# Kernel tuning notes

Measured on AMD Instinct MI355X. Metric: run time of the kernel, lower is better.

## Reference

```python
import jax, jax.numpy as jnp
import numpy as np

N = 8192
D = 256  # hidden_size = in_features = out_features
NEG_SLOPE = 0.01  # nn.LeakyReLU() default
MASK_VAL = -1e12


def setup_inputs() -> dict:
    key = jax.random.key(0)
    k1, k2, k3, k4 = jax.random.split(key, 4)
    x = jax.random.normal(k1, (N, D), dtype=jnp.float32)
    adj = jax.random.randint(k2, (N, N), 0, 2, dtype=jnp.int32)
    # kaiming_uniform_ style params (scaled random uniform)
    W = jax.random.normal(k3, (D, D), dtype=jnp.float32) * (1.0 / np.sqrt(D))
    a = jax.random.normal(k4, (2 * D, 1), dtype=jnp.float32) * (1.0 / np.sqrt(2 * D))
    return {"x": x, "adj": adj, "W": W, "a": a}


def reference(x, adj, W, a):
    # GraphAttentionLayer.forward (eval mode: dropout is identity)
    h = x @ W  # [N, D]
    # a_input[i,j] = concat(h_i, h_j); a_input @ a decomposes as:
    #   e[i,j] = h_i . a[:D] + h_j . a[D:]
    # identical math without materializing the [N, N, 2D] tensor.
    e_src = h @ a[:D, 0]  # [N]
    e_dst = h @ a[D:, 0]  # [N]
    e = e_src[:, None] + e_dst[None, :]  # [N, N]
    e = jnp.where(e > 0, e, NEG_SLOPE * e)  # LeakyReLU
    att_logits = jnp.where(adj > 0, e, MASK_VAL)
    attention = jax.nn.softmax(att_logits, axis=1)
    h_prime = attention @ h  # [N, D]
    return jax.nn.elu(h_prime)  # concat=True branch
```

## Files before the change

### kernel.cpp

```cpp
#include <hip/hip_runtime.h>

#define NN 8192
#define DD 256
#define JSPLIT 2
#define JCH (NN / JSPLIT)
#define NSTEP (JCH / 32)

typedef __attribute__((ext_vector_type(8))) short short8;
typedef __attribute__((ext_vector_type(4))) float f32x4;

__device__ __forceinline__ short f2bf(float x) {
    union { float f; unsigned u; } v; v.f = x;
    unsigned r = (v.u + 0x7FFFu + ((v.u >> 16) & 1u)) >> 16;
    return (short)r;
}
__device__ __forceinline__ float bf2f(short b) {
    union { float f; unsigned u; } v; v.u = ((unsigned)(unsigned short)b) << 16;
    return v.f;
}

__device__ __forceinline__ void barrier_keep_vmem() {
    asm volatile("s_waitcnt lgkmcnt(0)" ::: "memory");
    __builtin_amdgcn_s_barrier();
    asm volatile("" ::: "memory");
}

__global__ __launch_bounds__(256) void gat_prep(
    const float* __restrict__ x, const float* __restrict__ W,
    const float* __restrict__ a,
    short* __restrict__ hT, float* __restrict__ e_src, float* __restrict__ e_dst)
{
    __shared__ float x_s[32][260];
    __shared__ float W_s[2][16][256];
    const int t  = threadIdx.x;
    const int ib = blockIdx.x * 32;

    #pragma unroll
    for (int rep = 0; rep < 8; ++rep) {
        int fi = rep * 256 + t;
        int r  = fi >> 6;
        int c4 = (fi & 63) * 4;
        float4 v = *(const float4*)(x + (size_t)(ib + r) * DD + c4);
        *(float4*)&x_s[r][c4] = v;
    }
    float4 wp[4];
    #pragma unroll
    for (int q = 0; q < 4; ++q) {
        int fi = q * 256 + t;
        wp[q] = *(const float4*)(W + (size_t)(fi >> 6) * DD + (fi & 63) * 4);
    }
    barrier_keep_vmem();

    const int il = t >> 3;
    const int dg = (t & 7) * 4;
    f32x4 acc[8];
    #pragma unroll
    for (int m = 0; m < 8; ++m) acc[m] = (f32x4){0.f, 0.f, 0.f, 0.f};

    for (int kc = 0; kc < 16; ++kc) {
        const int b = kc & 1;
        #pragma unroll
        for (int q = 0; q < 4; ++q) {
            int fi = q * 256 + t;
            *(float4*)&W_s[b][fi >> 6][(fi & 63) * 4] = wp[q];
        }
        if (kc < 15) {
            #pragma unroll
            for (int q = 0; q < 4; ++q) {
                int fi = q * 256 + t;
                wp[q] = *(const float4*)(W + (size_t)((kc + 1) * 16 + (fi >> 6)) * DD + (fi & 63) * 4);
            }
        }
        barrier_keep_vmem();
        #pragma unroll
        for (int kl = 0; kl < 16; ++kl) {
            float xv = x_s[il][kc * 16 + kl];
            #pragma unroll
            for (int m = 0; m < 8; ++m) {
                float4 wv = *(const float4*)&W_s[b][kl][m * 32 + dg];
                acc[m].x += xv * wv.x; acc[m].y += xv * wv.y;
                acc[m].z += xv * wv.z; acc[m].w += xv * wv.w;
            }
        }
    }

    const int ig = ib + il;
    float p1 = 0.f, p2 = 0.f;
    #pragma unroll
    for (int m = 0; m < 8; ++m) {
        #pragma unroll
        for (int j = 0; j < 4; ++j) {
            int col = m * 32 + dg + j;
            float hv = acc[m][j];
            p1 += hv * a[col];
            p2 += hv * a[DD + col];
            hT[(size_t)col * NN + ig] = f2bf(hv);
        }
    }
    p1 += __shfl_xor(p1, 1); p1 += __shfl_xor(p1, 2); p1 += __shfl_xor(p1, 4);
    p2 += __shfl_xor(p2, 1); p2 += __shfl_xor(p2, 2); p2 += __shfl_xor(p2, 4);
    if ((t & 7) == 0) { e_src[ig] = p1; e_dst[ig] = p2; }
}

__global__ __launch_bounds__(512, 4) void gat_main(
    const int* __restrict__ adj, const short* __restrict__ hT,
    const float* __restrict__ e_src, const float* __restrict__ e_dst,
    float* __restrict__ num0, float* __restrict__ num1,
    float* __restrict__ den_part)
{
    __shared__ __align__(16) short w_s[2][32][40];

    const int t    = threadIdx.x;
    const int lane = t & 63;
    const int wid  = t >> 6;
    const int ibl  = (blockIdx.x >> 1) * 32;
    const int half = blockIdx.x & 1;
    const int jb   = half * JCH;

    const int irow = t >> 4;
    const int jc2  = (t & 15) * 2;
    const float es = e_src[ibl + irow];
    const int* adj_row = adj + (size_t)(ibl + irow) * NN + jb;
    const float* edp = e_dst + jb;

    const int cb   = wid * 32;
    const int arow = lane & 15;
    const int kg8  = (lane >> 4) * 8;
    const short* hB = hT + (size_t)(cb + arow) * NN + jb + kg8;

    float dsum = 0.f;
    f32x4 acc00 = {0.f,0.f,0.f,0.f}, acc01 = acc00, acc10 = acc00, acc11 = acc00;

    int2   adA = *(const int2*)(adj_row + jc2);
    float2 edA = *(const float2*)(edp + jc2);
    int4   b0A = *(const int4*)(hB);
    int4   b1A = *(const int4*)(hB + 16 * NN);
    int2   adB = *(const int2*)(adj_row + 32 + jc2);
    float2 edB = *(const float2*)(edp + 32 + jc2);
    int4   b0B = *(const int4*)(hB + 32);
    int4   b1B = *(const int4*)(hB + 16 * NN + 32);

#define MAIN_STEP(AD, ED, B0, B1, n)                                           \
    {                                                                          \
        const int c = (n) & 1;                                                 \
        int4 g0 = B0, g1 = B1;                       \
        float s0 = es + ED.x, s1 = es + ED.y;                                  \
        float l0 = s0 > 0.f ? s0 : 0.01f * s0;                                 \
        float l1 = s1 > 0.f ? s1 : 0.01f * s1;                                 \
        float w0 = AD.x > 0 ? __expf(l0) : 0.f;                                \
        float w1 = AD.y > 0 ? __expf(l1) : 0.f;                                \
        short b0 = f2bf(w0), b1 = f2bf(w1);                                    \
        dsum += bf2f(b0) + bf2f(b1);    \
        *(unsigned*)&w_s[c][irow][jc2] =                                       \
            (unsigned)(unsigned short)b0 | ((unsigned)(unsigned short)b1 << 16);\
        int jn = (((n) + 2) & (NSTEP - 1)) * 32;         \
        AD = *(const int2*)(adj_row + jn + jc2);                               \
        ED = *(const float2*)(edp + jn + jc2);                                 \
        B0 = *(const int4*)(hB + jn);                                          \
        B1 = *(const int4*)(hB + 16 * NN + jn);                                \
        barrier_keep_vmem();          \
        short8 a0 = *(const short8*)&w_s[c][arow][kg8];                        \
        short8 a1 = *(const short8*)&w_s[c][16 + arow][kg8];                   \
        acc00 = __builtin_amdgcn_mfma_f32_16x16x32_bf16(a0, *(short8*)&g0, acc00, 0, 0, 0);\
        acc01 = __builtin_amdgcn_mfma_f32_16x16x32_bf16(a0, *(short8*)&g1, acc01, 0, 0, 0);\
        acc10 = __builtin_amdgcn_mfma_f32_16x16x32_bf16(a1, *(short8*)&g0, acc10, 0, 0, 0);\
        acc11 = __builtin_amdgcn_mfma_f32_16x16x32_bf16(a1, *(short8*)&g1, acc11, 0, 0, 0);\
    }

    for (int n = 0; n < NSTEP; n += 2) {
        MAIN_STEP(adA, edA, b0A, b1A, n)
        MAIN_STEP(adB, edB, b0B, b1B, n + 1)
    }
#undef MAIN_STEP

    dsum += __shfl_xor(dsum, 1);
    dsum += __shfl_xor(dsum, 2);
    dsum += __shfl_xor(dsum, 4);
    dsum += __shfl_xor(dsum, 8);
    if ((t & 15) == 0) den_part[half * NN + ibl + irow] = dsum;

    float* num = half ? num1 : num0;
    const int r4 = (lane >> 4) * 4;
    #pragma unroll
    for (int r = 0; r < 4; ++r) {
        size_t o0 = (size_t)(ibl + r4 + r) * DD + cb + arow;
        size_t o1 = (size_t)(ibl + 16 + r4 + r) * DD + cb + arow;
        num[o0]      = acc00[r];
        num[o0 + 16] = acc01[r];
        num[o1]      = acc10[r];
        num[o1 + 16] = acc11[r];
    }
}

__global__ __launch_bounds__(256) void gat_epi(
    float* __restrict__ out, const float* __restrict__ num1,
    const float* __restrict__ den_part)
{
    int idx = blockIdx.x * 256 + threadIdx.x;
    int row = idx >> 6;
    float inv = 1.f / (den_part[row] + den_part[NN + row]);
    float4 p0 = ((const float4*)out)[idx];
    float4 p1 = ((const float4*)num1)[idx];
    float4 v;
    v.x = (p0.x + p1.x) * inv; v.x = v.x > 0.f ? v.x : expm1f(v.x);
    v.y = (p0.y + p1.y) * inv; v.y = v.y > 0.f ? v.y : expm1f(v.y);
    v.z = (p0.z + p1.z) * inv; v.z = v.z > 0.f ? v.z : expm1f(v.z);
    v.w = (p0.w + p1.w) * inv; v.w = v.w > 0.f ? v.w : expm1f(v.w);
    ((float4*)out)[idx] = v;
}

extern "C" void kernel_launch(void* const* d_in, const int* in_sizes, int n_in,
                              void* d_out, int out_size, void* d_ws, size_t ws_size,
                              hipStream_t stream) {
    const float* x   = (const float*)d_in[0];
    const int*   adj = (const int*)d_in[1];
    const float* W   = (const float*)d_in[2];
    const float* a   = (const float*)d_in[3];
    float* out = (float*)d_out;

    char* w0 = (char*)d_ws;
    short* hT   = (short*)w0;
    float* esrc = (float*)(w0 + (size_t)DD * NN * 2);
    float* edst = esrc + NN;
    float* den  = edst + NN;
    float* num1 = den + 2 * NN;

    gat_prep<<<dim3(NN / 32), dim3(256), 0, stream>>>(x, W, a, hT, esrc, edst);
    gat_main<<<dim3((NN / 32) * JSPLIT), dim3(512), 0, stream>>>(
        adj, hT, esrc, edst, out, num1, den);
    gat_epi<<<dim3(NN * DD / 4 / 256), dim3(256), 0, stream>>>(out, num1, den);
}
```

Measured before the change: 225.3 us.

## Bit-pack adjacency in a pre-pass, drop J-split and fuse normalization epilogue

A new kernel packs the int32 adjacency matrix into a 1-bit-per-edge mask. The main kernel then reads one mask word per 32 columns instead of streaming int32 adjacency values in its inner loop. The J split is removed, so each block handles full rows. That lets the softmax denominator and ELU be applied in the main kernel's epilogue, removing the partial-sum buffers and the separate epilogue kernel. The trade-offs are an extra full pass over adjacency and half as many main-kernel blocks, which lowers latency hiding in the MFMA loop.

```diff
diff --git a/kernel.cpp b/kernel.cpp
--- a/kernel.cpp
+++ b/kernel.cpp
@@ -2,9 +2,7 @@
 
 #define NN 8192
 #define DD 256
-#define JSPLIT 2
-#define JCH (NN / JSPLIT)
-#define NSTEP (JCH / 32)
+#define NSTEP (NN / 32)
 
 typedef __attribute__((ext_vector_type(8))) short short8;
 typedef __attribute__((ext_vector_type(4))) float f32x4;
@@ -23,6 +21,27 @@
     asm volatile("s_waitcnt lgkmcnt(0)" ::: "memory");
     __builtin_amdgcn_s_barrier();
     asm volatile("" ::: "memory");
+}
+
+__global__ __launch_bounds__(256) void gat_pack(
+    const int* __restrict__ adj, unsigned* __restrict__ bits)
+{
+    const int t   = threadIdx.x;
+    const int row = blockIdx.x;
+    const int* ar = adj + (size_t)row * NN;
+    unsigned* br  = bits + (size_t)row * (NN / 32);
+    #pragma unroll
+    for (int i = 0; i < 8; ++i) {
+        int j0 = i * 1024 + t * 4;
+        int4 v = *(const int4*)(ar + j0);
+        unsigned nib = (v.x > 0 ? 1u : 0u) | (v.y > 0 ? 2u : 0u)
+                     | (v.z > 0 ? 4u : 0u) | (v.w > 0 ? 8u : 0u);
+        unsigned word = nib << ((t & 7) * 4);
+        word |= __shfl_xor((int)word, 1);
+        word |= __shfl_xor((int)word, 2);
+        word |= __shfl_xor((int)word, 4);
+        if ((t & 7) == 0) br[i * 32 + (t >> 3)] = word;
+    }
 }
 
 __global__ __launch_bounds__(256) void gat_prep(
@@ -102,60 +121,57 @@
     if ((t & 7) == 0) { e_src[ig] = p1; e_dst[ig] = p2; }
 }
 
-__global__ __launch_bounds__(512, 4) void gat_main(
-    const int* __restrict__ adj, const short* __restrict__ hT,
+__global__ __launch_bounds__(512) void gat_main(
+    const unsigned* __restrict__ bits, const short* __restrict__ hT,
     const float* __restrict__ e_src, const float* __restrict__ e_dst,
-    float* __restrict__ num0, float* __restrict__ num1,
-    float* __restrict__ den_part)
+    float* __restrict__ out)
 {
     __shared__ __align__(16) short w_s[2][32][40];
+    __shared__ float denom_s[32];
 
     const int t    = threadIdx.x;
     const int lane = t & 63;
     const int wid  = t >> 6;
-    const int ibl  = (blockIdx.x >> 1) * 32;
-    const int half = blockIdx.x & 1;
-    const int jb   = half * JCH;
+    const int ibl  = blockIdx.x * 32;
 
     const int irow = t >> 4;
     const int jc2  = (t & 15) * 2;
     const float es = e_src[ibl + irow];
-    const int* adj_row = adj + (size_t)(ibl + irow) * NN + jb;
-    const float* edp = e_dst + jb;
+    const unsigned* bits_row = bits + (size_t)(ibl + irow) * (NN / 32);
 
     const int cb   = wid * 32;
     const int arow = lane & 15;
     const int kg8  = (lane >> 4) * 8;
-    const short* hB = hT + (size_t)(cb + arow) * NN + jb + kg8;
+    const short* hB = hT + (size_t)(cb + arow) * NN + kg8;
 
     float dsum = 0.f;
     f32x4 acc00 = {0.f,0.f,0.f,0.f}, acc01 = acc00, acc10 = acc00, acc11 = acc00;
 
-    int2   adA = *(const int2*)(adj_row + jc2);
-    float2 edA = *(const float2*)(edp + jc2);
-    int4   b0A = *(const int4*)(hB);
-    int4   b1A = *(const int4*)(hB + 16 * NN);
-    int2   adB = *(const int2*)(adj_row + 32 + jc2);
-    float2 edB = *(const float2*)(edp + 32 + jc2);
-    int4   b0B = *(const int4*)(hB + 32);
-    int4   b1B = *(const int4*)(hB + 16 * NN + 32);
-
-#define MAIN_STEP(AD, ED, B0, B1, n)                                           \
+    unsigned bwA = bits_row[0];
+    float2   edA = *(const float2*)(e_dst + jc2);
+    int4     b0A = *(const int4*)(hB);
+    int4     b1A = *(const int4*)(hB + 16 * NN);
+    unsigned bwB = bits_row[1];
+    float2   edB = *(const float2*)(e_dst + 32 + jc2);
+    int4     b0B = *(const int4*)(hB + 32);
+    int4     b1B = *(const int4*)(hB + 16 * NN + 32);
+
+#define MAIN_STEP(BW, ED, B0, B1, n)                                           \
     {                                                                          \
         const int c = (n) & 1;                                                 \
         int4 g0 = B0, g1 = B1;                       \
         float s0 = es + ED.x, s1 = es + ED.y;                                  \
         float l0 = s0 > 0.f ? s0 : 0.01f * s0;                                 \
         float l1 = s1 > 0.f ? s1 : 0.01f * s1;                                 \
-        float w0 = AD.x > 0 ? __expf(l0) : 0.f;                                \
-        float w1 = AD.y > 0 ? __expf(l1) : 0.f;                                \
+        float w0 = ((BW >> jc2) & 1u)       ? __expf(l0) : 0.f;                \
+        float w1 = ((BW >> (jc2 + 1)) & 1u) ? __expf(l1) : 0.f;                \
         short b0 = f2bf(w0), b1 = f2bf(w1);                                    \
         dsum += bf2f(b0) + bf2f(b1);    \
         *(unsigned*)&w_s[c][irow][jc2] =                                       \
             (unsigned)(unsigned short)b0 | ((unsigned)(unsigned short)b1 << 16);\
         int jn = (((n) + 2) & (NSTEP - 1)) * 32;         \
-        AD = *(const int2*)(adj_row + jn + jc2);                               \
-        ED = *(const float2*)(edp + jn + jc2);                                 \
+        BW = bits_row[jn >> 5];                                                \
+        ED = *(const float2*)(e_dst + jn + jc2);                               \
         B0 = *(const int4*)(hB + jn);                                          \
         B1 = *(const int4*)(hB + 16 * NN + jn);                                \
         barrier_keep_vmem();          \
@@ -168,8 +184,8 @@
     }
 
     for (int n = 0; n < NSTEP; n += 2) {
-        MAIN_STEP(adA, edA, b0A, b1A, n)
-        MAIN_STEP(adB, edB, b0B, b1B, n + 1)
+        MAIN_STEP(bwA, edA, b0A, b1A, n)
+        MAIN_STEP(bwB, edB, b0B, b1B, n + 1)
     }
 #undef MAIN_STEP
 
@@ -177,36 +193,25 @@
     dsum += __shfl_xor(dsum, 2);
     dsum += __shfl_xor(dsum, 4);
     dsum += __shfl_xor(dsum, 8);
-    if ((t & 15) == 0) den_part[half * NN + ibl + irow] = dsum;
-
-    float* num = half ? num1 : num0;
+    if ((t & 15) == 0) denom_s[irow] = dsum;
+    __syncthreads();
+
     const int r4 = (lane >> 4) * 4;
     #pragma unroll
     for (int r = 0; r < 4; ++r) {
+        float inv0 = 1.f / denom_s[r4 + r];
+        float inv1 = 1.f / denom_s[16 + r4 + r];
         size_t o0 = (size_t)(ibl + r4 + r) * DD + cb + arow;
         size_t o1 = (size_t)(ibl + 16 + r4 + r) * DD + cb + arow;
-        num[o0]      = acc00[r];
-        num[o0 + 16] = acc01[r];
-        num[o1]      = acc10[r];
-        num[o1 + 16] = acc11[r];
-    }
-}
-
-__global__ __launch_bounds__(256) void gat_epi(
-    float* __restrict__ out, const float* __restrict__ num1,
-    const float* __restrict__ den_part)
-{
-    int idx = blockIdx.x * 256 + threadIdx.x;
-    int row = idx >> 6;
-    float inv = 1.f / (den_part[row] + den_part[NN + row]);
-    float4 p0 = ((const float4*)out)[idx];
-    float4 p1 = ((const float4*)num1)[idx];
-    float4 v;
-    v.x = (p0.x + p1.x) * inv; v.x = v.x > 0.f ? v.x : expm1f(v.x);
-    v.y = (p0.y + p1.y) * inv; v.y = v.y > 0.f ? v.y : expm1f(v.y);
-    v.z = (p0.z + p1.z) * inv; v.z = v.z > 0.f ? v.z : expm1f(v.z);
-    v.w = (p0.w + p1.w) * inv; v.w = v.w > 0.f ? v.w : expm1f(v.w);
-    ((float4*)out)[idx] = v;
+        float v00 = acc00[r] * inv0; v00 = v00 > 0.f ? v00 : expm1f(v00);
+        float v01 = acc01[r] * inv0; v01 = v01 > 0.f ? v01 : expm1f(v01);
+        float v10 = acc10[r] * inv1; v10 = v10 > 0.f ? v10 : expm1f(v10);
+        float v11 = acc11[r] * inv1; v11 = v11 > 0.f ? v11 : expm1f(v11);
+        out[o0]      = v00;
+        out[o0 + 16] = v01;
+        out[o1]      = v10;
+        out[o1 + 16] = v11;
+    }
 }
 
 extern "C" void kernel_launch(void* const* d_in, const int* in_sizes, int n_in,
@@ -219,14 +224,12 @@
     float* out = (float*)d_out;
 
     char* w0 = (char*)d_ws;
-    short* hT   = (short*)w0;
-    float* esrc = (float*)(w0 + (size_t)DD * NN * 2);
-    float* edst = esrc + NN;
-    float* den  = edst + NN;
-    float* num1 = den + 2 * NN;
-
+    short* hT      = (short*)w0;
+    float* esrc    = (float*)(w0 + (size_t)DD * NN * 2);
+    float* edst    = esrc + NN;
+    unsigned* bits = (unsigned*)(edst + NN);
+
+    gat_pack<<<dim3(NN), dim3(256), 0, stream>>>(adj, bits);
     gat_prep<<<dim3(NN / 32), dim3(256), 0, stream>>>(x, W, a, hT, esrc, edst);
-    gat_main<<<dim3((NN / 32) * JSPLIT), dim3(512), 0, stream>>>(
-        adj, hT, esrc, edst, out, num1, den);
-    gat_epi<<<dim3(NN * DD / 4 / 256), dim3(256), 0, stream>>>(out, num1, den);
-}
+    gat_main<<<dim3(NN / 32), dim3(512), 0, stream>>>(bits, hT, esrc, edst, out);
+}
```

Result: no change. 221.3 us (-1.8%).
